# Kernel tuning notes

Hardware: AMD Instinct MI355X
Metric: run time of the kernel (lower is better)

The kernel has to match this reference:

```python
import jax, jax.numpy as jnp
import numpy as np

HIDDEN = 512
HEADS = 8
DHEAD = HIDDEN // HEADS  # 64


def setup_inputs() -> dict:
    key = jax.random.key(0)
    ks = jax.random.split(key, 12)
    B, S = 2, 2048
    inp = {
        "q": jax.random.normal(ks[0], (B, S, HIDDEN), dtype=jnp.float32),
        "k": jax.random.normal(ks[1], (B, S, HIDDEN), dtype=jnp.float32),
        "v": jax.random.normal(ks[2], (B, S, HIDDEN), dtype=jnp.float32),
        "mask": jnp.zeros((B, 1, 1, S), dtype=bool),
    }
    scale = 1.0 / np.sqrt(HIDDEN)
    for i, name in enumerate(["Wq", "Wk", "Wv", "Wm"]):
        inp[name] = jax.random.normal(ks[3 + i], (HIDDEN, HIDDEN), dtype=jnp.float32) * scale
    for i, name in enumerate(["bq", "bk", "bv", "bm"]):
        inp[name] = jax.random.normal(ks[7 + i], (HIDDEN,), dtype=jnp.float32) * 0.01
    return inp


def reference(q, k, v, mask, Wq, Wk, Wv, Wm, bq, bk, bv, bm):
    B = q.shape[0]
    # Linear projections (torch Linear: x @ W.T + b)
    qh = (jnp.einsum("bsd,ed->bse", q, Wq) + bq).reshape(B, HEADS, -1, DHEAD)
    kh = (jnp.einsum("bsd,ed->bse", k, Wk) + bk).reshape(B, HEADS, -1, DHEAD)
    vh = (jnp.einsum("bsd,ed->bse", v, Wv) + bv).reshape(B, HEADS, -1, DHEAD)
    # NOTE: the original module reshapes [B,S,512] -> [B,8,S',64] directly
    # (splitting the sequence dim into heads, not the hidden dim); replicated here.
    s = jnp.einsum("bhqd,bhkd->bhqk", qh, kh) / jnp.sqrt(jnp.float32(DHEAD))
    s = jnp.where(mask, jnp.float32(-1e9), s)
    s = jax.nn.softmax(s, axis=-1)
    # dropout is identity in eval mode
    attn = jnp.einsum("bhqk,bhkd->bhqd", s, vh)  # [B,H,S',64]
    attn = attn.transpose(0, 2, 1, 3).reshape(B, -1, HIDDEN)
    return jnp.einsum("bsd,ed->bse", attn, Wm) + bm
```

## Files before the change

### kernel.cpp

```cpp
#include <hip/hip_runtime.h>
#include <hip/hip_bf16.h>
#include <math.h>

typedef float  f32x4 __attribute__((ext_vector_type(4)));
typedef short  s16x8 __attribute__((ext_vector_type(8)));
typedef short  s16x4 __attribute__((ext_vector_type(4)));
typedef unsigned short u16x4 __attribute__((ext_vector_type(4)));

__device__ inline unsigned short bfc(float f){
  __hip_bfloat16 h = __float2bfloat16(f);
  unsigned short u; __builtin_memcpy(&u, &h, 2); return u;
}

__device__ inline f32x4 mfma16(s16x4 a, s16x4 b, f32x4 c){
#if __has_builtin(__builtin_amdgcn_mfma_f32_16x16x16_bf16)
  return __builtin_amdgcn_mfma_f32_16x16x16_bf16(a, b, c, 0, 0, 0);
#elif __has_builtin(__builtin_amdgcn_mfma_f32_16x16x16bf16_1k)
  return __builtin_amdgcn_mfma_f32_16x16x16bf16_1k(a, b, c, 0, 0, 0);
#else
  asm("v_mfma_f32_16x16x16_bf16 %0, %1, %2, %0" : "+v"(c) : "v"(a), "v"(b));
  return c;
#endif
}

__device__ inline void gl_lds16(const unsigned short* g, unsigned short* l){
  __builtin_amdgcn_global_load_lds(
      (const __attribute__((address_space(1))) unsigned int*)g,
      (__attribute__((address_space(3))) unsigned int*)l, 16, 0, 0);
}

__global__ __launch_bounds__(256) void prep(const float* __restrict__ q, const float* __restrict__ k,
                                            const float* __restrict__ v,
                                            const float* __restrict__ w0, const float* __restrict__ w1,
                                            const float* __restrict__ w2, const float* __restrict__ w3,
                                            const unsigned char* __restrict__ mask,
                                            unsigned short* __restrict__ AP, unsigned short* __restrict__ WP,
                                            float* __restrict__ mf){
  int y = blockIdx.y;
  int t = blockIdx.x * 256 + threadIdx.x;
  if (y < 3){
    const float* src = y==0 ? q : (y==1 ? k : v);
    unsigned short* d = AP + (size_t)y * 2097152;
    int r = t >> 6, g = t & 63;
    const float* sp = src + (size_t)r * 512 + g * 8;
    f32x4 a0 = *(const f32x4*)sp;
    f32x4 a1 = *(const f32x4*)(sp + 4);
    s16x8 o = { (short)bfc(a0.x),(short)bfc(a0.y),(short)bfc(a0.z),(short)bfc(a0.w),
                (short)bfc(a1.x),(short)bfc(a1.y),(short)bfc(a1.z),(short)bfc(a1.w) };
    size_t off = ((size_t)(((r>>4)*16 + (g>>2))*64 + (g&3)*16 + (r&15))) * 8;
    *(s16x8*)(d + off) = o;
  } else if (y < 7){
    if (blockIdx.x < 128){
      int yy = y - 3;
      const float* src = yy==0 ? w0 : yy==1 ? w1 : yy==2 ? w2 : w3;
      int c = t >> 6, g = t & 63;
      const float* sp = src + (size_t)c * 512 + g * 8;
      f32x4 a0 = *(const f32x4*)sp;
      f32x4 a1 = *(const f32x4*)(sp + 4);
      s16x8 o = { (short)bfc(a0.x),(short)bfc(a0.y),(short)bfc(a0.z),(short)bfc(a0.w),
                  (short)bfc(a1.x),(short)bfc(a1.y),(short)bfc(a1.z),(short)bfc(a1.w) };
      size_t off = ((size_t)(((c>>4)*16 + (g>>2))*64 + (g&3)*16 + (c&15))) * 8;
      *(s16x8*)(WP + yy*262144 + off) = o;
    }
  } else if (t < 4096){
    mf[t] = mask[t] ? -1.442695e9f : 0.0f;
  }
}

__global__ __launch_bounds__(256) void proj_gemm(const unsigned short* __restrict__ Ap,
    const unsigned short* __restrict__ Wp,
    const float* __restrict__ bq, const float* __restrict__ bk, const float* __restrict__ bv,
    unsigned short* __restrict__ pout){
  int z = blockIdx.z;
  const unsigned short* A = Ap + (size_t)z * 2097152;
  const unsigned short* W = Wp + (size_t)z * 262144;
  const float* bias = z==0 ? bq : (z==1 ? bk : bv);
  unsigned short* out = pout + (size_t)z * 2097152;

  int w = threadIdx.x >> 6, lane = threadIdx.x & 63;
  int lr = lane & 15, lg = lane >> 4;
  int rt = blockIdx.x * 4 + w;
  int bn = blockIdx.y;

  f32x4 acc[4] = {};
  const unsigned short* Abase = A + ((size_t)rt*8192 + lane*8);
  const unsigned short* Wbase = W + ((size_t)bn*32768 + lane*8);
#pragma unroll 4
  for (int kc = 0; kc < 16; ++kc){
    s16x8 af = *(const s16x8*)(Abase + kc*512);
#pragma unroll
    for (int n = 0; n < 4; ++n){
      s16x8 bf = *(const s16x8*)(Wbase + ((size_t)n*16 + kc)*512);
      acc[n] = __builtin_amdgcn_mfma_f32_16x16x32_bf16(af, bf, acc[n], 0, 0, 0);
    }
  }
  int orow = rt*16 + lg*4;
#pragma unroll
  for (int n = 0; n < 4; ++n){
    int col = bn*64 + n*16 + lr;
    float bv_ = bias[col];
#pragma unroll
    for (int r = 0; r < 4; ++r)
      out[(size_t)(orow + r)*512 + col] = bfc(acc[n][r] + bv_);
  }
}

__global__ __launch_bounds__(256) void vtrans(const unsigned short* __restrict__ Pv,
                                              unsigned short* __restrict__ Vt){
  int kt = blockIdx.x, bh = blockIdx.y;
  int b = bh >> 3, h = bh & 7;
  __shared__ unsigned short t[64][65];
  const unsigned short* src = Pv + (size_t)(b*2048 + h*256)*512 + kt*4096;
  for (int i = threadIdx.x; i < 4096; i += 256){ int r = i >> 6, c = i & 63; t[r][c] = src[i]; }
  __syncthreads();
  unsigned short* dst = Vt + (size_t)bh*131072 + kt*64;
  for (int i = threadIdx.x; i < 4096; i += 256){ int d = i >> 6, kk = i & 63; dst[(size_t)d*2048 + kk] = t[kk][d]; }
}

__global__ __launch_bounds__(256) void flash(const unsigned short* __restrict__ Pq,
                                             const unsigned short* __restrict__ Pk,
                                             const unsigned short* __restrict__ Vt,
                                             const float* __restrict__ mf,
                                             unsigned short* __restrict__ aout){
  int qt = blockIdx.x;
  int bh = blockIdx.y;
  int b = bh >> 3, h = bh & 7;
  int w = threadIdx.x >> 6;
  int wq = w & 1, wk = w >> 1;
  int lane = threadIdx.x & 63;
  int lr = lane & 15, lg = lane >> 4;

  const unsigned short* Qh  = Pq + (size_t)(b*2048 + h*256)*512;
  const unsigned short* Kh  = Pk + (size_t)(b*2048 + h*256)*512 + (size_t)wk*65536;
  const unsigned short* Vth = Vt + (size_t)bh*131072 + wk*1024;
  const float* mrow = mf + b*2048 + wk*1024;

  __shared__ char smem[65536];
  unsigned short* ktile = (unsigned short*)smem;
  unsigned short* vtile = (unsigned short*)(smem + 32768);
  float* obuf = (float*)smem;
  float* mlb  = (float*)(smem + 16384);

  int lrow = lane >> 3;
  int lcol = ((lane & 7) ^ lrow) * 8;

  s16x8 qf[2][2];
#pragma unroll
  for (int qq = 0; qq < 2; ++qq){
    int qrow = qt*64 + wq*32 + qq*16 + lr;
    qf[qq][0] = *(const s16x8*)(Qh + (size_t)qrow*64 + lg*8);
    qf[qq][1] = *(const s16x8*)(Qh + (size_t)qrow*64 + 32 + lg*8);
  }

  float m2[2] = {-INFINITY, -INFINITY}, l[2] = {0.f, 0.f};
  f32x4 accT[2][4] = {};
  int swz = (lr & 7) * 16;

#define STAGE(dbuf, kk0) { \
    unsigned short* kd = ktile + ((dbuf)*2 + wk)*4096; \
    unsigned short* vd = vtile + ((dbuf)*2 + wk)*4096; \
    _Pragma("unroll") \
    for (int ii = 0; ii < 4; ++ii){ \
      int i = wq*4 + ii; \
      gl_lds16(Kh  + (size_t)((kk0) + 8*i + lrow)*64 + lcol, kd + i*512); \
      gl_lds16(Vth + (size_t)(8*i + lrow)*2048 + (kk0) + lcol, vd + i*512); \
    } }

  STAGE(0, 0)
  __syncthreads();
  int cur = 0;

  for (int t = 0; t < 16; ++t){
    int k0 = t * 64;
    if (t < 15) STAGE(cur ^ 1, k0 + 64)

    const char* kb = (const char*)(ktile + (cur*2 + wk)*4096);
    const char* vb = (const char*)(vtile + (cur*2 + wk)*4096);

    float s2[2][4][4];
    __builtin_amdgcn_s_setprio(1);
#pragma unroll
    for (int n = 0; n < 4; ++n){
      int krow = n*16 + lr;
      s16x8 kf0 = *(const s16x8*)(kb + krow*128 + ((lg*16) ^ swz));
      s16x8 kf1 = *(const s16x8*)(kb + krow*128 + ((64 + lg*16) ^ swz));
      f32x4 mv = *(const f32x4*)(mrow + k0 + n*16 + lg*4);
#pragma unroll
      for (int qq = 0; qq < 2; ++qq){
        f32x4 a = {};
        a = __builtin_amdgcn_mfma_f32_16x16x32_bf16(kf0, qf[qq][0], a, 0, 0, 0);
        a = __builtin_amdgcn_mfma_f32_16x16x32_bf16(kf1, qf[qq][1], a, 0, 0, 0);
#pragma unroll
        for (int r = 0; r < 4; ++r)
          s2[qq][n][r] = __builtin_fmaf(a[r], 0.18033688f, mv[r]);
      }
    }
    __builtin_amdgcn_s_setprio(0);

    s16x4 pf[2][4];
#pragma unroll
    for (int qq = 0; qq < 2; ++qq){
      float t0 = fmaxf(fmaxf(s2[qq][0][0], s2[qq][0][1]), fmaxf(s2[qq][0][2], s2[qq][0][3]));
      float t1 = fmaxf(fmaxf(s2[qq][1][0], s2[qq][1][1]), fmaxf(s2[qq][1][2], s2[qq][1][3]));
      float t2 = fmaxf(fmaxf(s2[qq][2][0], s2[qq][2][1]), fmaxf(s2[qq][2][2], s2[qq][2][3]));
      float t3 = fmaxf(fmaxf(s2[qq][3][0], s2[qq][3][1]), fmaxf(s2[qq][3][2], s2[qq][3][3]));
      float rm = fmaxf(fmaxf(t0, t1), fmaxf(t2, t3));
      rm = fmaxf(rm, __shfl_xor(rm, 16));
      rm = fmaxf(rm, __shfl_xor(rm, 32));
      if (!__all(rm <= m2[qq] + 11.54f)){
        float mn = fmaxf(m2[qq], rm);
        float al = __builtin_amdgcn_exp2f(m2[qq] - mn);
        l[qq] *= al;
#pragma unroll
        for (int nd = 0; nd < 4; ++nd)
#pragma unroll
          for (int r = 0; r < 4; ++r) accT[qq][nd][r] *= al;
        m2[qq] = mn;
      }
#pragma unroll
      for (int n = 0; n < 4; ++n){
        float p0 = __builtin_amdgcn_exp2f(s2[qq][n][0] - m2[qq]);
        float p1 = __builtin_amdgcn_exp2f(s2[qq][n][1] - m2[qq]);
        float p2 = __builtin_amdgcn_exp2f(s2[qq][n][2] - m2[qq]);
        float p3 = __builtin_amdgcn_exp2f(s2[qq][n][3] - m2[qq]);
        l[qq] += (p0 + p1) + (p2 + p3);
        pf[qq][n] = (s16x4){ (short)bfc(p0), (short)bfc(p1), (short)bfc(p2), (short)bfc(p3) };
      }
    }

    __builtin_amdgcn_s_setprio(1);
#pragma unroll
    for (int n = 0; n < 4; ++n){
#pragma unroll
      for (int nd = 0; nd < 4; ++nd){
        int vrow = nd*16 + lr;
        s16x4 vf = *(const s16x4*)(vb + vrow*128 + ((n*32 + lg*8) ^ swz));
        accT[0][nd] = mfma16(vf, pf[0][n], accT[0][nd]);
        accT[1][nd] = mfma16(vf, pf[1][n], accT[1][nd]);
      }
    }
    __builtin_amdgcn_s_setprio(0);

    __syncthreads();
    cur ^= 1;
  }
#undef STAGE

  float lt[2];
#pragma unroll
  for (int qq = 0; qq < 2; ++qq){
    float x = l[qq] + __shfl_xor(l[qq], 16);
    lt[qq] = x + __shfl_xor(x, 32);
  }

  if (wk == 1){
#pragma unroll
    for (int qq = 0; qq < 2; ++qq){
      int wb2 = wq*2 + qq;
      if (lg == 0){ mlb[wb2*16 + lr] = m2[qq]; mlb[64 + wb2*16 + lr] = lt[qq]; }
#pragma unroll
      for (int nd = 0; nd < 4; ++nd)
        *(f32x4*)&obuf[((size_t)wb2*64 + lane)*16 + nd*4] = accT[qq][nd];
    }
  }
  __syncthreads();
  if (wk == 0){
#pragma unroll
    for (int qq = 0; qq < 2; ++qq){
      int wb2 = wq*2 + qq;
      float m1 = mlb[wb2*16 + lr];
      float l1 = mlb[64 + wb2*16 + lr];
      float mM = fmaxf(m2[qq], m1);
      float a0 = __builtin_amdgcn_exp2f(m2[qq] - mM);
      float a1 = __builtin_amdgcn_exp2f(m1 - mM);
      float inv = 1.f / (lt[qq]*a0 + l1*a1);
      int q = qt*64 + wq*32 + qq*16 + lr;
      int rt = (b*2048 + q) >> 4;
#pragma unroll
      for (int nd = 0; nd < 4; ++nd){
        f32x4 o1 = *(const f32x4*)&obuf[((size_t)wb2*64 + lane)*16 + nd*4];
        int g = h*8 + nd*2 + (lg >> 1);
        u16x4 ov;
#pragma unroll
        for (int r = 0; r < 4; ++r)
          ov[r] = bfc((accT[qq][nd][r]*a0 + o1[r]*a1) * inv);
        unsigned short* dp = aout + ((size_t)((rt*16 + (g>>2))*64 + (g&3)*16 + lr))*8 + (lg&1)*4;
        *(u16x4*)dp = ov;
      }
    }
  }
}

__global__ __launch_bounds__(256) void gemm_out(const unsigned short* __restrict__ Ap,
                                                const unsigned short* __restrict__ Wp,
                                                const float* __restrict__ bias,
                                                float* __restrict__ out){
  int w = threadIdx.x >> 6, lane = threadIdx.x & 63;
  int lr = lane & 15, lg = lane >> 4;
  int rt = blockIdx.x * 4 + w;
  int bn = blockIdx.y;
  f32x4 acc[4] = {};
  const unsigned short* Abase = Ap + ((size_t)rt*8192 + lane*8);
  const unsigned short* Wbase = Wp + ((size_t)bn*32768 + lane*8);
#pragma unroll 4
  for (int kc = 0; kc < 16; ++kc){
    s16x8 af = *(const s16x8*)(Abase + kc*512);
#pragma unroll
    for (int n = 0; n < 4; ++n){
      s16x8 bf = *(const s16x8*)(Wbase + ((size_t)n*16 + kc)*512);
      acc[n] = __builtin_amdgcn_mfma_f32_16x16x32_bf16(af, bf, acc[n], 0, 0, 0);
    }
  }
  int orow = rt*16 + lg*4;
#pragma unroll
  for (int n = 0; n < 4; ++n){
    int col = bn*64 + n*16 + lr;
    float bv_ = bias[col];
#pragma unroll
    for (int r = 0; r < 4; ++r)
      out[(size_t)(orow + r)*512 + col] = acc[n][r] + bv_;
  }
}

extern "C" void kernel_launch(void* const* d_in, const int* in_sizes, int n_in,
                              void* d_out, int out_size, void* d_ws, size_t ws_size,
                              hipStream_t stream) {
  const float* q  = (const float*)d_in[0];
  const float* k  = (const float*)d_in[1];
  const float* v  = (const float*)d_in[2];
  const unsigned char* mask = (const unsigned char*)d_in[3];
  const float* Wq = (const float*)d_in[4];
  const float* Wk = (const float*)d_in[5];
  const float* Wv = (const float*)d_in[6];
  const float* Wm = (const float*)d_in[7];
  const float* bq = (const float*)d_in[8];
  const float* bk = (const float*)d_in[9];
  const float* bv = (const float*)d_in[10];
  const float* bm = (const float*)d_in[11];

  unsigned short* ws = (unsigned short*)d_ws;
  unsigned short* WP   = ws;
  float*          MF   = (float*)(ws + 1048576);
  unsigned short* AP   = ws + 1056768;
  unsigned short* PQ   = ws + 7348224;
  unsigned short* VT   = ws + 13639680;
  unsigned short* AO   = ws + 15736832;

  prep<<<dim3(1024, 8), 256, 0, stream>>>(q, k, v, Wq, Wk, Wv, Wm, mask, AP, WP, MF);
  proj_gemm<<<dim3(64, 8, 3), 256, 0, stream>>>(AP, WP, bq, bk, bv, PQ);
  vtrans<<<dim3(32, 16), 256, 0, stream>>>(PQ + 2*2097152, VT);
  flash<<<dim3(32, 16), 256, 0, stream>>>(PQ, PQ + 2097152, VT, MF, AO);
  gemm_out<<<dim3(64, 8), 256, 0, stream>>>(AO, WP + 3*262144, bm, (float*)d_out);
}
```

Measured before the change: 85.49 us.

## Split flash-attention keys across four waves per query pair with 512-thread blocks

Doubles the flash kernel block to 512 threads, so each of four key-split wave groups handles 512 keys in 32-key tiles instead of two groups with 1024 keys in 64-key tiles. The LDS staging layout and swizzle for K and V tiles are adjusted to the smaller tiles, and the final merge now combines three partial softmax states through shared memory. The aim is more waves per block and more latency hiding, at the cost of twice as many loop barriers, a larger merge epilogue, and per-wave register limits from the launch bounds.

```diff
diff --git a/kernel.cpp b/kernel.cpp
--- a/kernel.cpp
+++ b/kernel.cpp
@@ -117,7 +117,7 @@
   for (int i = threadIdx.x; i < 4096; i += 256){ int d = i >> 6, kk = i & 63; dst[(size_t)d*2048 + kk] = t[kk][d]; }
 }
 
-__global__ __launch_bounds__(256) void flash(const unsigned short* __restrict__ Pq,
+__global__ __launch_bounds__(512, 4) void flash(const unsigned short* __restrict__ Pq,
                                              const unsigned short* __restrict__ Pk,
                                              const unsigned short* __restrict__ Vt,
                                              const float* __restrict__ mf,
@@ -131,18 +131,20 @@
   int lr = lane & 15, lg = lane >> 4;
 
   const unsigned short* Qh  = Pq + (size_t)(b*2048 + h*256)*512;
-  const unsigned short* Kh  = Pk + (size_t)(b*2048 + h*256)*512 + (size_t)wk*65536;
-  const unsigned short* Vth = Vt + (size_t)bh*131072 + wk*1024;
-  const float* mrow = mf + b*2048 + wk*1024;
+  const unsigned short* Kh  = Pk + (size_t)(b*2048 + h*256)*512 + (size_t)wk*32768;
+  const unsigned short* Vth = Vt + (size_t)bh*131072 + wk*512;
+  const float* mrow = mf + b*2048 + wk*512;
 
   __shared__ char smem[65536];
   unsigned short* ktile = (unsigned short*)smem;
   unsigned short* vtile = (unsigned short*)(smem + 32768);
   float* obuf = (float*)smem;
-  float* mlb  = (float*)(smem + 16384);
-
-  int lrow = lane >> 3;
-  int lcol = ((lane & 7) ^ lrow) * 8;
+  float* mlb  = (float*)(smem + 49152);
+
+  int krow_l = lane >> 3;
+  int kcol_l = ((lane & 7) ^ krow_l) * 8;
+  int vrow_l = lane >> 2;
+  int vcol_l = ((lane & 3) ^ (vrow_l & 3)) * 8;
 
   s16x8 qf[2][2];
 #pragma unroll
@@ -154,16 +156,17 @@
 
   float m2[2] = {-INFINITY, -INFINITY}, l[2] = {0.f, 0.f};
   f32x4 accT[2][4] = {};
-  int swz = (lr & 7) * 16;
+  int kswz = (lr & 7) * 16;
+  int vswz = (lr & 3) * 16;
 
 #define STAGE(dbuf, kk0) { \
-    unsigned short* kd = ktile + ((dbuf)*2 + wk)*4096; \
-    unsigned short* vd = vtile + ((dbuf)*2 + wk)*4096; \
+    unsigned short* kd = ktile + ((dbuf)*4 + wk)*2048; \
+    unsigned short* vd = vtile + ((dbuf)*4 + wk)*2048; \
     _Pragma("unroll") \
-    for (int ii = 0; ii < 4; ++ii){ \
-      int i = wq*4 + ii; \
-      gl_lds16(Kh  + (size_t)((kk0) + 8*i + lrow)*64 + lcol, kd + i*512); \
-      gl_lds16(Vth + (size_t)(8*i + lrow)*2048 + (kk0) + lcol, vd + i*512); \
+    for (int ii = 0; ii < 2; ++ii){ \
+      int i = wq*2 + ii; \
+      gl_lds16(Kh  + (size_t)((kk0) + 8*i + krow_l)*64 + kcol_l, kd + i*512); \
+      gl_lds16(Vth + (size_t)(16*i + vrow_l)*2048 + (kk0) + vcol_l, vd + i*512); \
     } }
 
   STAGE(0, 0)
@@ -171,19 +174,19 @@
   int cur = 0;
 
   for (int t = 0; t < 16; ++t){
-    int k0 = t * 64;
-    if (t < 15) STAGE(cur ^ 1, k0 + 64)
-
-    const char* kb = (const char*)(ktile + (cur*2 + wk)*4096);
-    const char* vb = (const char*)(vtile + (cur*2 + wk)*4096);
-
-    float s2[2][4][4];
+    int k0 = t * 32;
+    if (t < 15) STAGE(cur ^ 1, k0 + 32)
+
+    const char* kb = (const char*)(ktile + (cur*4 + wk)*2048);
+    const char* vb = (const char*)(vtile + (cur*4 + wk)*2048);
+
+    float s2[2][2][4];
     __builtin_amdgcn_s_setprio(1);
 #pragma unroll
-    for (int n = 0; n < 4; ++n){
+    for (int n = 0; n < 2; ++n){
       int krow = n*16 + lr;
-      s16x8 kf0 = *(const s16x8*)(kb + krow*128 + ((lg*16) ^ swz));
-      s16x8 kf1 = *(const s16x8*)(kb + krow*128 + ((64 + lg*16) ^ swz));
+      s16x8 kf0 = *(const s16x8*)(kb + krow*128 + ((lg*16) ^ kswz));
+      s16x8 kf1 = *(const s16x8*)(kb + krow*128 + ((64 + lg*16) ^ kswz));
       f32x4 mv = *(const f32x4*)(mrow + k0 + n*16 + lg*4);
 #pragma unroll
       for (int qq = 0; qq < 2; ++qq){
@@ -197,14 +200,12 @@
     }
     __builtin_amdgcn_s_setprio(0);
 
-    s16x4 pf[2][4];
+    s16x4 pf[2][2];
 #pragma unroll
     for (int qq = 0; qq < 2; ++qq){
       float t0 = fmaxf(fmaxf(s2[qq][0][0], s2[qq][0][1]), fmaxf(s2[qq][0][2], s2[qq][0][3]));
       float t1 = fmaxf(fmaxf(s2[qq][1][0], s2[qq][1][1]), fmaxf(s2[qq][1][2], s2[qq][1][3]));
-      float t2 = fmaxf(fmaxf(s2[qq][2][0], s2[qq][2][1]), fmaxf(s2[qq][2][2], s2[qq][2][3]));
-      float t3 = fmaxf(fmaxf(s2[qq][3][0], s2[qq][3][1]), fmaxf(s2[qq][3][2], s2[qq][3][3]));
-      float rm = fmaxf(fmaxf(t0, t1), fmaxf(t2, t3));
+      float rm = fmaxf(t0, t1);
       rm = fmaxf(rm, __shfl_xor(rm, 16));
       rm = fmaxf(rm, __shfl_xor(rm, 32));
       if (!__all(rm <= m2[qq] + 11.54f)){
@@ -218,7 +219,7 @@
         m2[qq] = mn;
       }
 #pragma unroll
-      for (int n = 0; n < 4; ++n){
+      for (int n = 0; n < 2; ++n){
         float p0 = __builtin_amdgcn_exp2f(s2[qq][n][0] - m2[qq]);
         float p1 = __builtin_amdgcn_exp2f(s2[qq][n][1] - m2[qq]);
         float p2 = __builtin_amdgcn_exp2f(s2[qq][n][2] - m2[qq]);
@@ -230,11 +231,11 @@
 
     __builtin_amdgcn_s_setprio(1);
 #pragma unroll
-    for (int n = 0; n < 4; ++n){
+    for (int n = 0; n < 2; ++n){
 #pragma unroll
       for (int nd = 0; nd < 4; ++nd){
         int vrow = nd*16 + lr;
-        s16x4 vf = *(const s16x4*)(vb + vrow*128 + ((n*32 + lg*8) ^ swz));
+        s16x4 vf = *(const s16x4*)(vb + vrow*64 + ((n*32 + lg*8) ^ vswz));
         accT[0][nd] = mfma16(vf, pf[0][n], accT[0][nd]);
         accT[1][nd] = mfma16(vf, pf[1][n], accT[1][nd]);
       }
@@ -253,37 +254,52 @@
     lt[qq] = x + __shfl_xor(x, 32);
   }
 
-  if (wk == 1){
+  if (wk != 0){
+    int j = wk - 1;
 #pragma unroll
     for (int qq = 0; qq < 2; ++qq){
-      int wb2 = wq*2 + qq;
-      if (lg == 0){ mlb[wb2*16 + lr] = m2[qq]; mlb[64 + wb2*16 + lr] = lt[qq]; }
+      int reg = j*4 + wq*2 + qq;
+      if (lg == 0){ mlb[reg*16 + lr] = m2[qq]; mlb[192 + reg*16 + lr] = lt[qq]; }
 #pragma unroll
       for (int nd = 0; nd < 4; ++nd)
-        *(f32x4*)&obuf[((size_t)wb2*64 + lane)*16 + nd*4] = accT[qq][nd];
+        *(f32x4*)&obuf[((size_t)reg*64 + lane)*16 + nd*4] = accT[qq][nd];
     }
   }
   __syncthreads();
   if (wk == 0){
 #pragma unroll
     for (int qq = 0; qq < 2; ++qq){
-      int wb2 = wq*2 + qq;
-      float m1 = mlb[wb2*16 + lr];
-      float l1 = mlb[64 + wb2*16 + lr];
-      float mM = fmaxf(m2[qq], m1);
+      float mj[3], lj[3];
+      float mM = m2[qq];
+#pragma unroll
+      for (int j = 0; j < 3; ++j){
+        int reg = j*4 + wq*2 + qq;
+        mj[j] = mlb[reg*16 + lr];
+        lj[j] = mlb[192 + reg*16 + lr];
+        mM = fmaxf(mM, mj[j]);
+      }
       float a0 = __builtin_amdgcn_exp2f(m2[qq] - mM);
-      float a1 = __builtin_amdgcn_exp2f(m1 - mM);
-      float inv = 1.f / (lt[qq]*a0 + l1*a1);
+      float aj[3];
+      float ltot = lt[qq] * a0;
+#pragma unroll
+      for (int j = 0; j < 3; ++j){
+        aj[j] = __builtin_amdgcn_exp2f(mj[j] - mM);
+        ltot += lj[j] * aj[j];
+      }
+      float inv = 1.f / ltot;
       int q = qt*64 + wq*32 + qq*16 + lr;
       int rt = (b*2048 + q) >> 4;
 #pragma unroll
       for (int nd = 0; nd < 4; ++nd){
-        f32x4 o1 = *(const f32x4*)&obuf[((size_t)wb2*64 + lane)*16 + nd*4];
+        f32x4 o = accT[qq][nd] * a0;
+#pragma unroll
+        for (int j = 0; j < 3; ++j){
+          int reg = j*4 + wq*2 + qq;
+          f32x4 oj = *(const f32x4*)&obuf[((size_t)reg*64 + lane)*16 + nd*4];
+          o += oj * aj[j];
+        }
         int g = h*8 + nd*2 + (lg >> 1);
-        u16x4 ov;
-#pragma unroll
-        for (int r = 0; r < 4; ++r)
-          ov[r] = bfc((accT[qq][nd][r]*a0 + o1[r]*a1) * inv);
+        u16x4 ov = { bfc(o[0]*inv), bfc(o[1]*inv), bfc(o[2]*inv), bfc(o[3]*inv) };
         unsigned short* dp = aout + ((size_t)((rt*16 + (g>>2))*64 + (g&3)*16 + lr))*8 + (lg&1)*4;
         *(u16x4*)dp = ov;
       }
@@ -349,6 +365,6 @@
   prep<<<dim3(1024, 8), 256, 0, stream>>>(q, k, v, Wq, Wk, Wv, Wm, mask, AP, WP, MF);
   proj_gemm<<<dim3(64, 8, 3), 256, 0, stream>>>(AP, WP, bq, bk, bv, PQ);
   vtrans<<<dim3(32, 16), 256, 0, stream>>>(PQ + 2*2097152, VT);
-  flash<<<dim3(32, 16), 256, 0, stream>>>(PQ, PQ + 2097152, VT, MF, AO);
+  flash<<<dim3(32, 16), 512, 0, stream>>>(PQ, PQ + 2097152, VT, MF, AO);
   gemm_out<<<dim3(64, 8), 256, 0, stream>>>(AO, WP + 3*262144, bm, (float*)d_out);
 }
```

After: 84.52 us. About the same (-1.1%).
